# Performance work log

Hardware: AMD Instinct MI355X
Metric: run time of the kernel (lower is better)

The kernel has to match this reference:

```python
import jax, jax.numpy as jnp
import numpy as np

N_NODES = 100000
N_EDGES = 1200000
D_IN = 64
D_OUT = 32
BN_EPS = 1e-5


def setup_inputs() -> dict:
    key = jax.random.key(0)
    ks = jax.random.split(key, 8)
    x = jax.random.normal(ks[0], (N_NODES, D_IN), dtype=jnp.float32)
    edge_index = jax.random.randint(ks[1], (2, N_EDGES), 0, N_NODES, dtype=jnp.int64)
    W1s = jax.random.normal(ks[2], (3, D_IN, D_IN), dtype=jnp.float32) * 0.05
    b1s = jax.random.normal(ks[3], (3, D_IN), dtype=jnp.float32) * 0.05
    W2s = jax.random.normal(ks[4], (3, D_IN, D_IN), dtype=jnp.float32) * 0.05
    b2s = jax.random.normal(ks[5], (3, D_IN), dtype=jnp.float32) * 0.05
    gammas = jnp.ones((3, D_IN), dtype=jnp.float32)
    betas = jnp.zeros((3, D_IN), dtype=jnp.float32)
    epss = jnp.zeros((3,), dtype=jnp.float32)  # GINConv train_eps init value 0
    lin_w = jax.random.normal(ks[6], (D_IN, D_OUT), dtype=jnp.float32) * 0.05
    lin_b = jnp.zeros((D_OUT,), dtype=jnp.float32)
    return {"x": x, "edge_index": edge_index, "W1s": W1s, "b1s": b1s,
            "W2s": W2s, "b2s": b2s, "gammas": gammas, "betas": betas,
            "epss": epss, "lin_w": lin_w, "lin_b": lin_b}


def reference(x, edge_index, W1s, b1s, W2s, b2s, gammas, betas, epss, lin_w, lin_b):
    # PyG GINConv (source_to_target): out_i = nn((1+eps)*x_i + sum_{j->i} x_j)
    src = edge_index[0]
    dst = edge_index[1]
    n = x.shape[0]
    h = x
    for i in range(3):
        agg = jax.ops.segment_sum(h[src], dst, num_segments=n)  # [N, d]
        z = (1.0 + epss[i]) * h + agg
        z = jax.nn.relu(z @ W1s[i] + b1s[i])
        z = jax.nn.relu(z @ W2s[i] + b2s[i])
        # BatchNorm1d, training mode (batch statistics, biased variance)
        mu = jnp.mean(z, axis=0)
        var = jnp.var(z, axis=0)
        z = gammas[i] * (z - mu) * jax.lax.rsqrt(var + BN_EPS) + betas[i]
        h = jax.nn.relu(z)  # F.relu after each conv
    return h @ lin_w + lin_b  # [N, D_OUT]
```

## Files before the change

### kernel.cpp

```cpp
#include <hip/hip_runtime.h>
#include <hip/hip_fp16.h>
#include <hip/hip_cooperative_groups.h>

#define NBMAX 256
#define BCAP  8192
#define CHB   3584

typedef _Float16 half8 __attribute__((ext_vector_type(8)));
typedef float f32x4 __attribute__((ext_vector_type(4)));

__device__ __forceinline__ unsigned short f2h(float f) {
    __half h = __float2half_rn(f);
    return *(unsigned short*)&h;
}

__device__ __forceinline__ int scan256(int v, int* wsum, int* woff) {
    int t = threadIdx.x, lane = t & 63, wv = t >> 6;
    int x = v;
    #pragma unroll
    for (int d = 1; d < 64; d <<= 1) {
        int y = __shfl_up(x, d, 64);
        if (lane >= d) x += y;
    }
    if (lane == 63) wsum[wv] = x;
    __syncthreads();
    if (t == 0) {
        int a = 0;
        #pragma unroll
        for (int i = 0; i < 4; ++i) { woff[i] = a; a += wsum[i]; }
    }
    __syncthreads();
    return x - v + woff[wv];
}

__global__ __launch_bounds__(256) void gin_prep(const float* __restrict__ x,
                                                unsigned short* __restrict__ o, int n16,
                                                const void* __restrict__ edge,
                                                int* __restrict__ gcount,
                                                uint2* __restrict__ ebuf,
                                                int E, int nb, int nbin) {
    if ((int)blockIdx.x >= nbin) {
        int i = (blockIdx.x - nbin) * 256 + threadIdx.x;
        if (i >= n16) return;
        float4 v = ((const float4*)x)[i];
        ushort4 u;
        u.x = f2h(v.x); u.y = f2h(v.y); u.z = f2h(v.z); u.w = f2h(v.w);
        ((ushort4*)o)[i] = u;
        return;
    }
    __shared__ int cnt[NBMAX];
    __shared__ int dlt[NBMAX];
    __shared__ int cur[NBMAX];
    __shared__ int wsum[4], woff[4];
    __shared__ int s_is64;
    __shared__ uint2 buf[CHB];
    int t = threadIdx.x;
    int beg = blockIdx.x * CHB;
    int m = E - beg; if (m > CHB) m = CHB;
    if (t < nb) cnt[t] = 0;
    if (t == 0) s_is64 = 1;
    __syncthreads();
    {
        int m2 = (E < 64) ? E : 64;
        if (t < m2 && ((const int*)edge)[2 * t + 1] != 0) s_is64 = 0;
    }
    __syncthreads();
    int is64 = s_is64;
    for (int j = t; j < m; j += 256) {
        int e = beg + j;
        int d = is64 ? (int)((const long long*)edge)[E + e] : ((const int*)edge)[E + e];
        atomicAdd(&cnt[d >> 9], 1);
    }
    __syncthreads();
    int v = (t < nb) ? cnt[t] : 0;
    int excl = scan256(v, wsum, woff);
    if (t < nb) {
        int gb = v ? atomicAdd(&gcount[t], v) : 0;
        dlt[t] = t * BCAP + gb - excl;
        cur[t] = excl;
    }
    __syncthreads();
    for (int j = t; j < m; j += 256) {
        int e = beg + j;
        int s, d;
        if (is64) {
            s = (int)((const long long*)edge)[e];
            d = (int)((const long long*)edge)[E + e];
        } else {
            s = ((const int*)edge)[e];
            d = ((const int*)edge)[E + e];
        }
        int p = atomicAdd(&cur[d >> 9], 1);
        buf[p] = make_uint2((unsigned)s, (unsigned)d);
    }
    __syncthreads();
    for (int j = t; j < m; j += 256) {
        uint2 ed = buf[j];
        ebuf[j + dlt[(int)(ed.y >> 9)]] = ed;
    }
}

__global__ __launch_bounds__(256) void gin_build(const uint2* __restrict__ ebuf,
                                                 const int* __restrict__ gcount,
                                                 int* __restrict__ rowbeg,
                                                 int* __restrict__ rowend,
                                                 int* __restrict__ col, int n) {
    __shared__ int cnt[512];
    __shared__ int off[512];
    __shared__ int wsum[4], woff[4];
    int b = blockIdx.x, t = threadIdx.x;
    int beg = b * BCAP;
    int end = beg + gcount[b];
    cnt[t] = 0; cnt[t + 256] = 0;
    __syncthreads();
    for (int j = beg + t; j < end; j += 256)
        atomicAdd(&cnt[(int)(ebuf[j].y & 511)], 1);
    __syncthreads();
    int v0 = cnt[2 * t], v1 = cnt[2 * t + 1];
    int ep = scan256(v0 + v1, wsum, woff);
    off[2 * t] = ep;
    off[2 * t + 1] = ep + v0;
    __syncthreads();
    int node0 = b * 512 + 2 * t;
    if (node0 < n) {
        rowbeg[node0] = beg + off[2 * t];
        rowend[node0] = beg + off[2 * t] + v0;
    }
    if (node0 + 1 < n) {
        rowbeg[node0 + 1] = beg + off[2 * t + 1];
        rowend[node0 + 1] = beg + off[2 * t + 1] + v1;
    }
    __syncthreads();
    for (int j = beg + t; j < end; j += 256) {
        uint2 ed = ebuf[j];
        int p = atomicAdd(&off[(int)(ed.y & 511)], 1);
        col[beg + p] = (int)ed.x;
    }
}

template <bool APPLY>
__device__ __forceinline__ void accum8(float* acc, uint4 u,
                                       const float* sc, const float* sh) {
    float v[8];
    float2 f;
    f = __half22float2(*(const __half2*)&u.x); v[0] = f.x; v[1] = f.y;
    f = __half22float2(*(const __half2*)&u.y); v[2] = f.x; v[3] = f.y;
    f = __half22float2(*(const __half2*)&u.z); v[4] = f.x; v[5] = f.y;
    f = __half22float2(*(const __half2*)&u.w); v[6] = f.x; v[7] = f.y;
    #pragma unroll
    for (int j = 0; j < 8; ++j)
        acc[j] += APPLY ? fmaxf(fmaf(v[j], sc[j], sh[j]), 0.f) : v[j];
}

template <bool APPLY>
__device__ __forceinline__ void gather_node(const unsigned short* __restrict__ zb,
                                            int r0, int r1, int ci0,
                                            const int* __restrict__ col,
                                            float e1,
                                            const float* sc, const float* sh,
                                            _Float16* __restrict__ trow,
                                            int wid, int qn, int l16) {
    int r = l16 >> 3, c = l16 & 7;
    uint4 su = make_uint4(0, 0, 0, 0);
    if (r == 0) su = *(const uint4*)(zb + (size_t)wid * 64 + 8 * c);

    float acc[8] = {0.f, 0.f, 0.f, 0.f, 0.f, 0.f, 0.f, 0.f};
    int ci = ci0;
    for (int b2 = r0; b2 < r1; b2 += 16) {
        if (b2 > r0) {
            int ce = b2 + l16;
            ci = col[ce < r1 ? ce : r1 - 1];
        }
        uint4 u[8];
        bool p[8];
        #pragma unroll
        for (int s = 0; s < 8; ++s) {
            int j = 2 * s + r;
            p[s] = (b2 + j) < r1;
            int idx = __shfl(ci, 16 * qn + j);
            if (p[s]) u[s] = *(const uint4*)(zb + (size_t)idx * 64 + 8 * c);
        }
        #pragma unroll
        for (int s = 0; s < 8; ++s)
            if (p[s]) accum8<APPLY>(acc, u[s], sc, sh);
    }
    #pragma unroll
    for (int j = 0; j < 8; ++j)
        acc[j] += __shfl_xor(acc[j], 8);
    if (r == 0) {
        float s[8];
        float2 f;
        f = __half22float2(*(const __half2*)&su.x); s[0] = f.x; s[1] = f.y;
        f = __half22float2(*(const __half2*)&su.y); s[2] = f.x; s[3] = f.y;
        f = __half22float2(*(const __half2*)&su.z); s[4] = f.x; s[5] = f.y;
        f = __half22float2(*(const __half2*)&su.w); s[6] = f.x; s[7] = f.y;
        #pragma unroll
        for (int j = 0; j < 8; ++j) {
            float v = APPLY ? fmaxf(fmaf(s[j], sc[j], sh[j]), 0.f) : s[j];
            acc[j] = fmaf(e1, v, acc[j]);
        }
        uint4 o;
        o.x = (unsigned)f2h(acc[0]) | ((unsigned)f2h(acc[1]) << 16);
        o.y = (unsigned)f2h(acc[2]) | ((unsigned)f2h(acc[3]) << 16);
        o.z = (unsigned)f2h(acc[4]) | ((unsigned)f2h(acc[5]) << 16);
        o.w = (unsigned)f2h(acc[6]) | ((unsigned)f2h(acc[7]) << 16);
        *(uint4*)(trow + 8 * c) = o;
    }
}

template <bool APPLY, bool FINAL>
__global__ __launch_bounds__(512, 4) void gin_fused(const unsigned short* __restrict__ zb,
                                                    const int* __restrict__ rowbeg,
                                                    const int* __restrict__ rowend,
                                                    const int* __restrict__ col,
                                                    const float* __restrict__ epss,
                                                    const float* __restrict__ gammas,
                                                    const float* __restrict__ betas,
                                                    float fN,
                                                    unsigned short* __restrict__ z16,
                                                    const float* __restrict__ W1g,
                                                    const float* __restrict__ b1g,
                                                    const float* __restrict__ W2g,
                                                    const float* __restrict__ b2g,
                                                    float* __restrict__ stats,
                                                    int layer, int n,
                                                    const float* __restrict__ lw,
                                                    const float* __restrict__ lb,
                                                    float* __restrict__ out) {
    __shared__ _Float16 Wt[2 * 64 * 72];
    __shared__ _Float16 Tz[128 * 72];
    __shared__ float sS[64], sQ[64];
    __shared__ float sBN[128];
    int tid = threadIdx.x;
    int base = blockIdx.x * 128;
    const float* __restrict__ W1 = W1g + layer * 4096;
    const float* __restrict__ W2 = W2g + layer * 4096;

    for (int i = tid; i < 4096; i += 512) {
        int k = i >> 6, nn = i & 63;
        Wt[nn * 72 + k]        = (_Float16)W1[i];
        Wt[4608 + nn * 72 + k] = (_Float16)W2[i];
    }
    if (tid < 64) {
        sS[tid] = 0.f; sQ[tid] = 0.f;
        if (APPLY) {
            float mu  = stats[(layer - 1) * 128 + tid] / fN;
            float var = stats[(layer - 1) * 128 + 64 + tid] / fN - mu * mu;
            float g   = gammas[(layer - 1) * 64 + tid];
            float grs = g * rsqrtf(var + 1e-5f);
            sBN[tid]      = grs;
            sBN[64 + tid] = betas[(layer - 1) * 64 + tid] - grs * mu;
        }
    }
    __syncthreads();

    int lane = tid & 63, wv = tid >> 6;
    int qn = lane >> 4;
    int l16 = lane & 15;
    int c8 = l16 & 7;
    float e1 = 1.f + epss[layer];
    float sc[8] = {1.f, 1.f, 1.f, 1.f, 1.f, 1.f, 1.f, 1.f};
    float sh[8] = {0.f, 0.f, 0.f, 0.f, 0.f, 0.f, 0.f, 0.f};
    if (APPLY) {
        *(float4*)&sc[0] = *(const float4*)&sBN[8 * c8];
        *(float4*)&sc[4] = *(const float4*)&sBN[8 * c8 + 4];
        *(float4*)&sh[0] = *(const float4*)&sBN[64 + 8 * c8];
        *(float4*)&sh[4] = *(const float4*)&sBN[64 + 8 * c8 + 4];
    }

    int wvq = wv * 4 + qn;
    int cr0, cr1, pr0, pr1;
    {
        int w0 = base + wvq;
        cr0 = 0; cr1 = 0;
        if (w0 < n) { cr0 = rowbeg[w0]; cr1 = rowend[w0]; }
        int w1 = w0 + 32;
        pr0 = 0; pr1 = 0;
        if (w1 < n) { pr0 = rowbeg[w1]; pr1 = rowend[w1]; }
    }
    int cci = 0;
    if (cr1 > cr0) { int ce = cr0 + l16; cci = col[ce < cr1 ? ce : cr1 - 1]; }
    #pragma unroll 1
    for (int p = 0; p < 4; ++p) {
        int nci = 0;
        if (pr1 > pr0) { int ce = pr0 + l16; nci = col[ce < pr1 ? ce : pr1 - 1]; }
        int fr0 = 0, fr1 = 0;
        {
            int w2 = base + (p + 2) * 32 + wvq;
            if (p < 2 && w2 < n) { fr0 = rowbeg[w2]; fr1 = rowend[w2]; }
        }
        int widl = p * 32 + wvq;
        int wid = base + widl;
        if (wid < n) {
            gather_node<APPLY>(zb, cr0, cr1, cci, col, e1, sc, sh,
                               Tz + widl * 72, wid, qn, l16);
        } else if (l16 < 8) {
            *(uint4*)(Tz + widl * 72 + 8 * c8) = make_uint4(0u, 0u, 0u, 0u);
        }
        cr0 = pr0; cr1 = pr1; cci = nci;
        pr0 = fr0; pr1 = fr1;
    }
    __syncthreads();

    int g = qn, q = l16;
    int n0 = 16 * wv + q;

    half8 tb0 = *(const half8*)&Tz[n0 * 72 + 8 * g];
    half8 tb1 = *(const half8*)&Tz[n0 * 72 + 32 + 8 * g];

    f32x4 acc[4];
    #pragma unroll
    for (int ft = 0; ft < 4; ++ft)
        acc[ft] = (f32x4){0.f, 0.f, 0.f, 0.f};

    #pragma unroll
    for (int ft = 0; ft < 4; ++ft) {
        half8 a0 = *(const half8*)&Wt[(16 * ft + q) * 72 + 8 * g];
        half8 a1 = *(const half8*)&Wt[(16 * ft + q) * 72 + 32 + 8 * g];
        acc[ft] = __builtin_amdgcn_mfma_f32_16x16x32_f16(a0, tb0, acc[ft], 0, 0, 0);
        acc[ft] = __builtin_amdgcn_mfma_f32_16x16x32_f16(a1, tb1, acc[ft], 0, 0, 0);
    }

    #pragma unroll
    for (int ft = 0; ft < 4; ++ft) {
        float4 b = *(const float4*)(b1g + layer * 64 + 16 * ft + 4 * g);
        float v0 = fmaxf(acc[ft][0] + b.x, 0.f);
        float v1 = fmaxf(acc[ft][1] + b.y, 0.f);
        float v2 = fmaxf(acc[ft][2] + b.z, 0.f);
        float v3 = fmaxf(acc[ft][3] + b.w, 0.f);
        uint2 pk;
        pk.x = (unsigned)f2h(v0) | ((unsigned)f2h(v1) << 16);
        pk.y = (unsigned)f2h(v2) | ((unsigned)f2h(v3) << 16);
        *(uint2*)&Tz[n0 * 72 + 16 * ft + 4 * g] = pk;
    }

    half8 zb0 = *(const half8*)&Tz[n0 * 72 + 8 * g];
    half8 zb1 = *(const half8*)&Tz[n0 * 72 + 32 + 8 * g];
    #pragma unroll
    for (int ft = 0; ft < 4; ++ft)
        acc[ft] = (f32x4){0.f, 0.f, 0.f, 0.f};
    #pragma unroll
    for (int ft = 0; ft < 4; ++ft) {
        half8 a0 = *(const half8*)&Wt[4608 + (16 * ft + q) * 72 + 8 * g];
        half8 a1 = *(const half8*)&Wt[4608 + (16 * ft + q) * 72 + 32 + 8 * g];
        acc[ft] = __builtin_amdgcn_mfma_f32_16x16x32_f16(a0, zb0, acc[ft], 0, 0, 0);
        acc[ft] = __builtin_amdgcn_mfma_f32_16x16x32_f16(a1, zb1, acc[ft], 0, 0, 0);
    }

    int nodeg = base + n0;
    #pragma unroll
    for (int ft = 0; ft < 4; ++ft) {
        float4 b = *(const float4*)(b2g + layer * 64 + 16 * ft + 4 * g);
        float v0 = fmaxf(acc[ft][0] + b.x, 0.f);
        float v1 = fmaxf(acc[ft][1] + b.y, 0.f);
        float v2 = fmaxf(acc[ft][2] + b.z, 0.f);
        float v3 = fmaxf(acc[ft][3] + b.w, 0.f);
        float s[4], sq[4];
        bool ok = nodeg < n;
        s[0] = ok ? v0 : 0.f; sq[0] = ok ? v0 * v0 : 0.f;
        s[1] = ok ? v1 : 0.f; sq[1] = ok ? v1 * v1 : 0.f;
        s[2] = ok ? v2 : 0.f; sq[2] = ok ? v2 * v2 : 0.f;
        s[3] = ok ? v3 : 0.f; sq[3] = ok ? v3 * v3 : 0.f;
        uint2 pk;
        pk.x = (unsigned)f2h(v0) | ((unsigned)f2h(v1) << 16);
        pk.y = (unsigned)f2h(v2) | ((unsigned)f2h(v3) << 16);
        *(uint2*)&Tz[n0 * 72 + 16 * ft + 4 * g] = pk;
        #pragma unroll
        for (int off = 1; off < 16; off <<= 1) {
            #pragma unroll
            for (int r2 = 0; r2 < 4; ++r2) {
                s[r2] += __shfl_xor(s[r2], off);
                sq[r2] += __shfl_xor(sq[r2], off);
            }
        }
        if (q == 0) {
            #pragma unroll
            for (int r2 = 0; r2 < 4; ++r2) {
                atomicAdd(&sS[16 * ft + 4 * g + r2], s[r2]);
                atomicAdd(&sQ[16 * ft + 4 * g + r2], sq[r2]);
            }
        }
    }

    if constexpr (!FINAL) {
        #pragma unroll
        for (int t2 = 0; t2 < 2; ++t2) {
            int u = lane + 64 * t2;
            int rloc = 16 * wv + (u >> 3);
            int node = base + rloc;
            if (node < n) {
                uint4 v = *(const uint4*)&Tz[rloc * 72 + (u & 7) * 8];
                *(uint4*)(z16 + (size_t)node * 64 + (u & 7) * 8) = v;
            }
        }
        __syncthreads();
        if (tid < 64) {
            atomicAdd(&stats[layer * 128 + tid], sS[tid]);
            atomicAdd(&stats[layer * 128 + 64 + tid], sQ[tid]);
        }
    } else {
        __syncthreads();
        if (tid < 64) {
            atomicAdd(&stats[layer * 128 + tid], sS[tid]);
            atomicAdd(&stats[layer * 128 + 64 + tid], sQ[tid]);
        }
        __threadfence();
        cooperative_groups::this_grid().sync();

        float* Wl = (float*)Wt;
        for (int i = tid; i < 2048; i += 512) Wl[i] = lw[i];
        if (tid < 64) {
            float mu  = stats[layer * 128 + tid] / fN;
            float var = stats[layer * 128 + 64 + tid] / fN - mu * mu;
            float g2  = gammas[layer * 64 + tid];
            float grs = g2 * rsqrtf(var + 1e-5f);
            sBN[tid]      = grs;
            sBN[64 + tid] = betas[layer * 64 + tid] - grs * mu;
        }
        __syncthreads();

        int tx = tid & 7, ty = tid >> 3;
        float accL[2][4];
        {
            float4 b = *(const float4*)(lb + 4 * tx);
            #pragma unroll
            for (int r = 0; r < 2; ++r) {
                accL[r][0] = b.x; accL[r][1] = b.y; accL[r][2] = b.z; accL[r][3] = b.w;
            }
        }
        #pragma unroll 4
        for (int k = 0; k < 64; ++k) {
            float4 w2 = *(const float4*)&Wl[k * 32 + 4 * tx];
            float s_ = sBN[k], h_ = sBN[64 + k];
            #pragma unroll
            for (int r = 0; r < 2; ++r) {
                int row = ty + 64 * r;
                float zv = (float)Tz[row * 72 + k];
                float a = fmaxf(fmaf(zv, s_, h_), 0.f);
                accL[r][0] = fmaf(a, w2.x, accL[r][0]);
                accL[r][1] = fmaf(a, w2.y, accL[r][1]);
                accL[r][2] = fmaf(a, w2.z, accL[r][2]);
                accL[r][3] = fmaf(a, w2.w, accL[r][3]);
            }
        }
        #pragma unroll
        for (int r = 0; r < 2; ++r) {
            int row = base + ty + 64 * r;
            if (row < n) {
                float4 v;
                v.x = accL[r][0]; v.y = accL[r][1]; v.z = accL[r][2]; v.w = accL[r][3];
                *(float4*)(out + (size_t)row * 32 + 4 * tx) = v;
            }
        }
    }
}

__global__ __launch_bounds__(256) void gin_lin(const unsigned short* __restrict__ zin,
                                               const float* __restrict__ stats,
                                               const float* __restrict__ gammas,
                                               const float* __restrict__ betas,
                                               float fN,
                                               const float* __restrict__ lw,
                                               const float* __restrict__ lb,
                                               float* __restrict__ out, int n) {
    __shared__ float Z[128 * 68];
    int tid = threadIdx.x;
    int base = blockIdx.x * 128;
    int cq = (tid & 15) * 4;
    float4 sc4, sh4;
    {
        float t0[4], t1[4];
        #pragma unroll
        for (int j = 0; j < 4; ++j) {
            int f = cq + j;
            float mu  = stats[256 + f] / fN;
            float var = stats[256 + 64 + f] / fN - mu * mu;
            float g   = gammas[128 + f];
            float grs = g * rsqrtf(var + 1e-5f);
            t0[j] = grs;
            t1[j] = betas[128 + f] - grs * mu;
        }
        sc4 = make_float4(t0[0], t0[1], t0[2], t0[3]);
        sh4 = make_float4(t1[0], t1[1], t1[2], t1[3]);
    }
    {
        const ushort4* __restrict__ src = (const ushort4*)(zin + (size_t)base * 64);
        #pragma unroll
        for (int it = 0; it < 8; ++it) {
            int idx4 = it * 256 + tid;
            int row = idx4 >> 4, c = (idx4 & 15) * 4;
            float4 v = make_float4(0.f, 0.f, 0.f, 0.f);
            if (base + row < n) {
                ushort4 u = src[idx4];
                float2 f0 = __half22float2(*(const __half2*)&u.x);
                float2 f1 = __half22float2(*(const __half2*)&u.z);
                v = make_float4(f0.x, f0.y, f1.x, f1.y);
            }
            float4 r;
            r.x = fmaxf(fmaf(v.x, sc4.x, sh4.x), 0.f);
            r.y = fmaxf(fmaf(v.y, sc4.y, sh4.y), 0.f);
            r.z = fmaxf(fmaf(v.z, sc4.z, sh4.z), 0.f);
            r.w = fmaxf(fmaf(v.w, sc4.w, sh4.w), 0.f);
            *(float4*)&Z[row * 68 + c] = r;
        }
    }
    __syncthreads();
    int tx = tid & 7, ty = tid >> 3;
    float acc[4][4];
    {
        float4 b = *(const float4*)(lb + 4 * tx);
        #pragma unroll
        for (int r = 0; r < 4; ++r) {
            acc[r][0] = b.x; acc[r][1] = b.y; acc[r][2] = b.z; acc[r][3] = b.w;
        }
    }
    #pragma unroll 4
    for (int k = 0; k < 64; ++k) {
        float4 w = *(const float4*)(lw + k * 32 + 4 * tx);
        #pragma unroll
        for (int r = 0; r < 4; ++r) {
            float a = Z[(ty + 32 * r) * 68 + k];
            acc[r][0] = fmaf(a, w.x, acc[r][0]);
            acc[r][1] = fmaf(a, w.y, acc[r][1]);
            acc[r][2] = fmaf(a, w.z, acc[r][2]);
            acc[r][3] = fmaf(a, w.w, acc[r][3]);
        }
    }
    #pragma unroll
    for (int r = 0; r < 4; ++r) {
        int row = base + ty + 32 * r;
        if (row < n) {
            float4 v;
            v.x = acc[r][0]; v.y = acc[r][1]; v.z = acc[r][2]; v.w = acc[r][3];
            *(float4*)(out + (size_t)row * 32 + 4 * tx) = v;
        }
    }
}

extern "C" void kernel_launch(void* const* d_in, const int* in_sizes, int n_in,
                              void* d_out, int out_size, void* d_ws, size_t ws_size,
                              hipStream_t stream) {
    const float* x      = (const float*)d_in[0];
    const void*  edge   = d_in[1];
    const float* W1s    = (const float*)d_in[2];
    const float* b1s    = (const float*)d_in[3];
    const float* W2s    = (const float*)d_in[4];
    const float* b2s    = (const float*)d_in[5];
    const float* gammas = (const float*)d_in[6];
    const float* betas  = (const float*)d_in[7];
    const float* epss   = (const float*)d_in[8];
    const float* lin_w  = (const float*)d_in[9];
    const float* lin_b  = (const float*)d_in[10];
    float* out = (float*)d_out;

    const int N = in_sizes[0] / 64;
    const int E = in_sizes[1] / 2;
    const int NB = (N + 511) >> 9;
    const float fN = (float)N;

    char* w = (char*)d_ws;
    auto take = [&](size_t bytes) {
        char* p = w;
        w += (bytes + 255) & ~(size_t)255;
        return p;
    };
    unsigned short* x16 = (unsigned short*)take((size_t)N * 64 * 2);
    unsigned short* hA  = (unsigned short*)take((size_t)N * 64 * 2);
    unsigned short* hB  = (unsigned short*)take((size_t)N * 64 * 2);
    uint2* ebuf    = (uint2*)take((size_t)NB * BCAP * 8);
    int*   col     = (int*)take((size_t)NB * BCAP * 4);
    int*   rowbeg  = (int*)take((size_t)N * 4);
    int*   rowend  = (int*)take((size_t)N * 4);
    int*   gcount  = (int*)take((size_t)NBMAX * 4);
    float* stats   = (float*)take(3 * 128 * 4);

    hipMemsetAsync(gcount, 0, 1024 + 1536, stream);

    const int n16 = N * 16;
    const int nbin = (E + CHB - 1) / CHB;
    const int gx = (n16 + 255) / 256;
    gin_prep<<<nbin + gx, 256, 0, stream>>>(x, x16, n16, edge, gcount, ebuf, E, NB, nbin);
    gin_build<<<NB, 256, 0, stream>>>(ebuf, gcount, rowbeg, rowend, col, N);

    const int gMlp = (N + 127) / 128;

    gin_fused<false, false><<<gMlp, 512, 0, stream>>>(x16, rowbeg, rowend, col, epss,
                                                      gammas, betas, fN, hA,
                                                      W1s, b1s, W2s, b2s, stats, 0, N,
                                                      nullptr, nullptr, nullptr);
    gin_fused<true, false><<<gMlp, 512, 0, stream>>>(hA, rowbeg, rowend, col, epss,
                                                     gammas, betas, fN, hB,
                                                     W1s, b1s, W2s, b2s, stats, 1, N,
                                                     nullptr, nullptr, nullptr);

    bool coop = false;
    {
        int dev = 0;
        hipGetDevice(&dev);
        int numCU = 0;
        hipDeviceGetAttribute(&numCU, hipDeviceAttributeMultiprocessorCount, dev);
        int maxB = 0;
        hipOccupancyMaxActiveBlocksPerMultiprocessor(
            &maxB, reinterpret_cast<const void*>(&gin_fused<true, true>), 512, 0);
        if (maxB > 0 && numCU > 0 && (long long)maxB * numCU >= (long long)gMlp)
            coop = true;
    }
    if (coop) {
        const unsigned short* zi = hB;
        unsigned short* zo = hA;
        int Lv = 2, Nv = N;
        float fNv = fN;
        void* args[] = {
            (void*)&zi, (void*)&rowbeg, (void*)&rowend, (void*)&col,
            (void*)&epss, (void*)&gammas, (void*)&betas, (void*)&fNv,
            (void*)&zo, (void*)&W1s, (void*)&b1s, (void*)&W2s, (void*)&b2s,
            (void*)&stats, (void*)&Lv, (void*)&Nv,
            (void*)&lin_w, (void*)&lin_b, (void*)&out
        };
        hipError_t err = hipLaunchCooperativeKernel(
            reinterpret_cast<const void*>(&gin_fused<true, true>),
            dim3(gMlp), dim3(512), args, 0, stream);
        if (err != hipSuccess) coop = false;
    }
    if (!coop) {
        gin_fused<true, false><<<gMlp, 512, 0, stream>>>(hB, rowbeg, rowend, col, epss,
                                                         gammas, betas, fN, hA,
                                                         W1s, b1s, W2s, b2s, stats, 2, N,
                                                         nullptr, nullptr, nullptr);
        gin_lin<<<gMlp, 256, 0, stream>>>(hA, stats, gammas, betas, fN, lin_w, lin_b, out, N);
    }
}
```

Baseline: 301.2 us.

## Fuse all three GIN layers and final linear into one persistent megakernel

Replaces the three per-layer kernel launches plus the cooperative final launch with a single persistent kernel. It loops over the layers and separates them with a custom atomic grid barrier in global memory, in place of cooperative-groups grid sync. The aim is to remove launch gaps and per-layer kernel tails. The barrier relies on every block being co-resident under a plain launch, checked only via an occupancy query, and launch_bounds is raised to 8 blocks per CU, which may constrain registers.

```diff
diff --git a/kernel.cpp b/kernel.cpp
--- a/kernel.cpp
+++ b/kernel.cpp
@@ -1,6 +1,5 @@
 #include <hip/hip_runtime.h>
 #include <hip/hip_fp16.h>
-#include <hip/hip_cooperative_groups.h>
 
 #define NBMAX 256
 #define BCAP  8192
@@ -208,7 +207,172 @@
     }
 }
 
-template <bool APPLY, bool FINAL>
+template <bool APPLY>
+__device__ __forceinline__ void gin_layer(const unsigned short* __restrict__ zb,
+                                          const int* __restrict__ rowbeg,
+                                          const int* __restrict__ rowend,
+                                          const int* __restrict__ col,
+                                          float e1,
+                                          const float* __restrict__ b1,
+                                          const float* __restrict__ b2,
+                                          float* __restrict__ statsL,
+                                          _Float16* __restrict__ Wt,
+                                          _Float16* __restrict__ Tz,
+                                          float* __restrict__ sS,
+                                          float* __restrict__ sQ,
+                                          const float* __restrict__ sBN,
+                                          int base, int n) {
+    int tid = threadIdx.x;
+    int lane = tid & 63, wv = tid >> 6;
+    int qn = lane >> 4;
+    int l16 = lane & 15;
+    int c8 = l16 & 7;
+    float sc[8] = {1.f, 1.f, 1.f, 1.f, 1.f, 1.f, 1.f, 1.f};
+    float sh[8] = {0.f, 0.f, 0.f, 0.f, 0.f, 0.f, 0.f, 0.f};
+    if (APPLY) {
+        *(float4*)&sc[0] = *(const float4*)&sBN[8 * c8];
+        *(float4*)&sc[4] = *(const float4*)&sBN[8 * c8 + 4];
+        *(float4*)&sh[0] = *(const float4*)&sBN[64 + 8 * c8];
+        *(float4*)&sh[4] = *(const float4*)&sBN[64 + 8 * c8 + 4];
+    }
+
+    int wvq = wv * 4 + qn;
+    int cr0, cr1, pr0, pr1;
+    {
+        int w0 = base + wvq;
+        cr0 = 0; cr1 = 0;
+        if (w0 < n) { cr0 = rowbeg[w0]; cr1 = rowend[w0]; }
+        int w1 = w0 + 32;
+        pr0 = 0; pr1 = 0;
+        if (w1 < n) { pr0 = rowbeg[w1]; pr1 = rowend[w1]; }
+    }
+    int cci = 0;
+    if (cr1 > cr0) { int ce = cr0 + l16; cci = col[ce < cr1 ? ce : cr1 - 1]; }
+    #pragma unroll 1
+    for (int p = 0; p < 4; ++p) {
+        int nci = 0;
+        if (pr1 > pr0) { int ce = pr0 + l16; nci = col[ce < pr1 ? ce : pr1 - 1]; }
+        int fr0 = 0, fr1 = 0;
+        {
+            int w2 = base + (p + 2) * 32 + wvq;
+            if (p < 2 && w2 < n) { fr0 = rowbeg[w2]; fr1 = rowend[w2]; }
+        }
+        int widl = p * 32 + wvq;
+        int wid = base + widl;
+        if (wid < n) {
+            gather_node<APPLY>(zb, cr0, cr1, cci, col, e1, sc, sh,
+                               Tz + widl * 72, wid, qn, l16);
+        } else if (l16 < 8) {
+            *(uint4*)(Tz + widl * 72 + 8 * c8) = make_uint4(0u, 0u, 0u, 0u);
+        }
+        cr0 = pr0; cr1 = pr1; cci = nci;
+        pr0 = fr0; pr1 = fr1;
+    }
+    __syncthreads();
+
+    int g = qn, q = l16;
+    int n0 = 16 * wv + q;
+
+    half8 tb0 = *(const half8*)&Tz[n0 * 72 + 8 * g];
+    half8 tb1 = *(const half8*)&Tz[n0 * 72 + 32 + 8 * g];
+
+    f32x4 acc[4];
+    #pragma unroll
+    for (int ft = 0; ft < 4; ++ft)
+        acc[ft] = (f32x4){0.f, 0.f, 0.f, 0.f};
+
+    #pragma unroll
+    for (int ft = 0; ft < 4; ++ft) {
+        half8 a0 = *(const half8*)&Wt[(16 * ft + q) * 72 + 8 * g];
+        half8 a1 = *(const half8*)&Wt[(16 * ft + q) * 72 + 32 + 8 * g];
+        acc[ft] = __builtin_amdgcn_mfma_f32_16x16x32_f16(a0, tb0, acc[ft], 0, 0, 0);
+        acc[ft] = __builtin_amdgcn_mfma_f32_16x16x32_f16(a1, tb1, acc[ft], 0, 0, 0);
+    }
+
+    #pragma unroll
+    for (int ft = 0; ft < 4; ++ft) {
+        float4 b = *(const float4*)(b1 + 16 * ft + 4 * g);
+        float v0 = fmaxf(acc[ft][0] + b.x, 0.f);
+        float v1 = fmaxf(acc[ft][1] + b.y, 0.f);
+        float v2 = fmaxf(acc[ft][2] + b.z, 0.f);
+        float v3 = fmaxf(acc[ft][3] + b.w, 0.f);
+        uint2 pk;
+        pk.x = (unsigned)f2h(v0) | ((unsigned)f2h(v1) << 16);
+        pk.y = (unsigned)f2h(v2) | ((unsigned)f2h(v3) << 16);
+        *(uint2*)&Tz[n0 * 72 + 16 * ft + 4 * g] = pk;
+    }
+
+    half8 zb0 = *(const half8*)&Tz[n0 * 72 + 8 * g];
+    half8 zb1 = *(const half8*)&Tz[n0 * 72 + 32 + 8 * g];
+    #pragma unroll
+    for (int ft = 0; ft < 4; ++ft)
+        acc[ft] = (f32x4){0.f, 0.f, 0.f, 0.f};
+    #pragma unroll
+    for (int ft = 0; ft < 4; ++ft) {
+        half8 a0 = *(const half8*)&Wt[4608 + (16 * ft + q) * 72 + 8 * g];
+        half8 a1 = *(const half8*)&Wt[4608 + (16 * ft + q) * 72 + 32 + 8 * g];
+        acc[ft] = __builtin_amdgcn_mfma_f32_16x16x32_f16(a0, zb0, acc[ft], 0, 0, 0);
+        acc[ft] = __builtin_amdgcn_mfma_f32_16x16x32_f16(a1, zb1, acc[ft], 0, 0, 0);
+    }
+
+    int nodeg = base + n0;
+    #pragma unroll
+    for (int ft = 0; ft < 4; ++ft) {
+        float4 b = *(const float4*)(b2 + 16 * ft + 4 * g);
+        float v0 = fmaxf(acc[ft][0] + b.x, 0.f);
+        float v1 = fmaxf(acc[ft][1] + b.y, 0.f);
+        float v2 = fmaxf(acc[ft][2] + b.z, 0.f);
+        float v3 = fmaxf(acc[ft][3] + b.w, 0.f);
+        float s[4], sq[4];
+        bool ok = nodeg < n;
+        s[0] = ok ? v0 : 0.f; sq[0] = ok ? v0 * v0 : 0.f;
+        s[1] = ok ? v1 : 0.f; sq[1] = ok ? v1 * v1 : 0.f;
+        s[2] = ok ? v2 : 0.f; sq[2] = ok ? v2 * v2 : 0.f;
+        s[3] = ok ? v3 : 0.f; sq[3] = ok ? v3 * v3 : 0.f;
+        uint2 pk;
+        pk.x = (unsigned)f2h(v0) | ((unsigned)f2h(v1) << 16);
+        pk.y = (unsigned)f2h(v2) | ((unsigned)f2h(v3) << 16);
+        *(uint2*)&Tz[n0 * 72 + 16 * ft + 4 * g] = pk;
+        #pragma unroll
+        for (int off = 1; off < 16; off <<= 1) {
+            #pragma unroll
+            for (int r2 = 0; r2 < 4; ++r2) {
+                s[r2] += __shfl_xor(s[r2], off);
+                sq[r2] += __shfl_xor(sq[r2], off);
+            }
+        }
+        if (q == 0) {
+            #pragma unroll
+            for (int r2 = 0; r2 < 4; ++r2) {
+                atomicAdd(&sS[16 * ft + 4 * g + r2], s[r2]);
+                atomicAdd(&sQ[16 * ft + 4 * g + r2], sq[r2]);
+            }
+        }
+    }
+    __syncthreads();
+    if (tid < 64) {
+        atomicAdd(&statsL[tid], sS[tid]);
+        atomicAdd(&statsL[64 + tid], sQ[tid]);
+    }
+}
+
+__device__ __forceinline__ void copyout_z16(const _Float16* __restrict__ Tz,
+                                            unsigned short* __restrict__ z16,
+                                            int base, int n) {
+    int lane = threadIdx.x & 63, wv = threadIdx.x >> 6;
+    #pragma unroll
+    for (int t2 = 0; t2 < 2; ++t2) {
+        int u = lane + 64 * t2;
+        int rloc = 16 * wv + (u >> 3);
+        int node = base + rloc;
+        if (node < n) {
+            uint4 v = *(const uint4*)&Tz[rloc * 72 + (u & 7) * 8];
+            *(uint4*)(z16 + (size_t)node * 64 + (u & 7) * 8) = v;
+        }
+    }
+}
+
+template <bool APPLY>
 __global__ __launch_bounds__(512, 4) void gin_fused(const unsigned short* __restrict__ zb,
                                                     const int* __restrict__ rowbeg,
                                                     const int* __restrict__ rowend,
@@ -223,10 +387,7 @@
                                                     const float* __restrict__ W2g,
                                                     const float* __restrict__ b2g,
                                                     float* __restrict__ stats,
-                                                    int layer, int n,
-                                                    const float* __restrict__ lw,
-                                                    const float* __restrict__ lb,
-                                                    float* __restrict__ out) {
+                                                    int layer, int n) {
     __shared__ _Float16 Wt[2 * 64 * 72];
     __shared__ _Float16 Tz[128 * 72];
     __shared__ float sS[64], sQ[64];
@@ -235,7 +396,6 @@
     int base = blockIdx.x * 128;
     const float* __restrict__ W1 = W1g + layer * 4096;
     const float* __restrict__ W2 = W2g + layer * 4096;
-
     for (int i = tid; i < 4096; i += 512) {
         int k = i >> 6, nn = i & 63;
         Wt[nn * 72 + k]        = (_Float16)W1[i];
@@ -253,204 +413,125 @@
         }
     }
     __syncthreads();
-
-    int lane = tid & 63, wv = tid >> 6;
-    int qn = lane >> 4;
-    int l16 = lane & 15;
-    int c8 = l16 & 7;
-    float e1 = 1.f + epss[layer];
-    float sc[8] = {1.f, 1.f, 1.f, 1.f, 1.f, 1.f, 1.f, 1.f};
-    float sh[8] = {0.f, 0.f, 0.f, 0.f, 0.f, 0.f, 0.f, 0.f};
-    if (APPLY) {
-        *(float4*)&sc[0] = *(const float4*)&sBN[8 * c8];
-        *(float4*)&sc[4] = *(const float4*)&sBN[8 * c8 + 4];
-        *(float4*)&sh[0] = *(const float4*)&sBN[64 + 8 * c8];
-        *(float4*)&sh[4] = *(const float4*)&sBN[64 + 8 * c8 + 4];
-    }
-
-    int wvq = wv * 4 + qn;
-    int cr0, cr1, pr0, pr1;
+    gin_layer<APPLY>(zb, rowbeg, rowend, col, 1.f + epss[layer],
+                     b1g + layer * 64, b2g + layer * 64, stats + layer * 128,
+                     Wt, Tz, sS, sQ, sBN, base, n);
+    copyout_z16(Tz, z16, base, n);
+}
+
+__device__ __forceinline__ void megabar(int* __restrict__ bar, int target) {
+    __syncthreads();
+    if (threadIdx.x == 0) {
+        __threadfence();
+        __hip_atomic_fetch_add(bar, 1, __ATOMIC_RELEASE, __HIP_MEMORY_SCOPE_AGENT);
+        while (__hip_atomic_load(bar, __ATOMIC_ACQUIRE, __HIP_MEMORY_SCOPE_AGENT) < target)
+            __builtin_amdgcn_s_sleep(16);
+    }
+    __syncthreads();
+    __threadfence();
+}
+
+__global__ __launch_bounds__(512, 8) void gin_mega(const unsigned short* __restrict__ x16,
+                                                   unsigned short* __restrict__ hA,
+                                                   unsigned short* __restrict__ hB,
+                                                   const int* __restrict__ rowbeg,
+                                                   const int* __restrict__ rowend,
+                                                   const int* __restrict__ col,
+                                                   const float* __restrict__ epss,
+                                                   const float* __restrict__ gammas,
+                                                   const float* __restrict__ betas,
+                                                   float fN,
+                                                   const float* __restrict__ W1g,
+                                                   const float* __restrict__ b1g,
+                                                   const float* __restrict__ W2g,
+                                                   const float* __restrict__ b2g,
+                                                   float* __restrict__ stats, int n,
+                                                   const float* __restrict__ lw,
+                                                   const float* __restrict__ lb,
+                                                   float* __restrict__ out,
+                                                   int* __restrict__ bar, int nblocks) {
+    __shared__ _Float16 Wt[2 * 64 * 72];
+    __shared__ _Float16 Tz[128 * 72];
+    __shared__ float sS[64], sQ[64];
+    __shared__ float sBN[128];
+    int tid = threadIdx.x;
+    int base = blockIdx.x * 128;
+
+    #pragma unroll 1
+    for (int L = 0; L < 3; ++L) {
+        const unsigned short* zb = (L == 0) ? x16 : ((L == 1) ? hA : hB);
+        const float* W1 = W1g + L * 4096;
+        const float* W2 = W2g + L * 4096;
+        for (int i = tid; i < 4096; i += 512) {
+            int k = i >> 6, nn = i & 63;
+            Wt[nn * 72 + k]        = (_Float16)W1[i];
+            Wt[4608 + nn * 72 + k] = (_Float16)W2[i];
+        }
+        if (tid < 64) {
+            sS[tid] = 0.f; sQ[tid] = 0.f;
+            if (L > 0) {
+                float mu  = stats[(L - 1) * 128 + tid] / fN;
+                float var = stats[(L - 1) * 128 + 64 + tid] / fN - mu * mu;
+                float g   = gammas[(L - 1) * 64 + tid];
+                float grs = g * rsqrtf(var + 1e-5f);
+                sBN[tid]      = grs;
+                sBN[64 + tid] = betas[(L - 1) * 64 + tid] - grs * mu;
+            }
+        }
+        __syncthreads();
+        float e1 = 1.f + epss[L];
+        if (L > 0)
+            gin_layer<true>(zb, rowbeg, rowend, col, e1, b1g + L * 64, b2g + L * 64,
+                            stats + L * 128, Wt, Tz, sS, sQ, sBN, base, n);
+        else
+            gin_layer<false>(zb, rowbeg, rowend, col, e1, b1g, b2g,
+                             stats, Wt, Tz, sS, sQ, sBN, base, n);
+        if (L < 2) copyout_z16(Tz, (L == 0) ? hA : hB, base, n);
+        megabar(bar, nblocks * (L + 1));
+    }
+
+    float* Wl = (float*)Wt;
+    for (int i = tid; i < 2048; i += 512) Wl[i] = lw[i];
+    if (tid < 64) {
+        float mu  = stats[256 + tid] / fN;
+        float var = stats[256 + 64 + tid] / fN - mu * mu;
+        float g2  = gammas[128 + tid];
+        float grs = g2 * rsqrtf(var + 1e-5f);
+        sBN[tid]      = grs;
+        sBN[64 + tid] = betas[128 + tid] - grs * mu;
+    }
+    __syncthreads();
+    int tx = tid & 7, ty = tid >> 3;
+    float accL[2][4];
     {
-        int w0 = base + wvq;
-        cr0 = 0; cr1 = 0;
-        if (w0 < n) { cr0 = rowbeg[w0]; cr1 = rowend[w0]; }
-        int w1 = w0 + 32;
-        pr0 = 0; pr1 = 0;
-        if (w1 < n) { pr0 = rowbeg[w1]; pr1 = rowend[w1]; }
-    }
-    int cci = 0;
-    if (cr1 > cr0) { int ce = cr0 + l16; cci = col[ce < cr1 ? ce : cr1 - 1]; }
-    #pragma unroll 1
-    for (int p = 0; p < 4; ++p) {
-        int nci = 0;
-        if (pr1 > pr0) { int ce = pr0 + l16; nci = col[ce < pr1 ? ce : pr1 - 1]; }
-        int fr0 = 0, fr1 = 0;
-        {
-            int w2 = base + (p + 2) * 32 + wvq;
-            if (p < 2 && w2 < n) { fr0 = rowbeg[w2]; fr1 = rowend[w2]; }
-        }
-        int widl = p * 32 + wvq;
-        int wid = base + widl;
-        if (wid < n) {
-            gather_node<APPLY>(zb, cr0, cr1, cci, col, e1, sc, sh,
-                               Tz + widl * 72, wid, qn, l16);
-        } else if (l16 < 8) {
-            *(uint4*)(Tz + widl * 72 + 8 * c8) = make_uint4(0u, 0u, 0u, 0u);
-        }
-        cr0 = pr0; cr1 = pr1; cci = nci;
-        pr0 = fr0; pr1 = fr1;
-    }
-    __syncthreads();
-
-    int g = qn, q = l16;
-    int n0 = 16 * wv + q;
-
-    half8 tb0 = *(const half8*)&Tz[n0 * 72 + 8 * g];
-    half8 tb1 = *(const half8*)&Tz[n0 * 72 + 32 + 8 * g];
-
-    f32x4 acc[4];
-    #pragma unroll
-    for (int ft = 0; ft < 4; ++ft)
-        acc[ft] = (f32x4){0.f, 0.f, 0.f, 0.f};
-
-    #pragma unroll
-    for (int ft = 0; ft < 4; ++ft) {
-        half8 a0 = *(const half8*)&Wt[(16 * ft + q) * 72 + 8 * g];
-        half8 a1 = *(const half8*)&Wt[(16 * ft + q) * 72 + 32 + 8 * g];
-        acc[ft] = __builtin_amdgcn_mfma_f32_16x16x32_f16(a0, tb0, acc[ft], 0, 0, 0);
-        acc[ft] = __builtin_amdgcn_mfma_f32_16x16x32_f16(a1, tb1, acc[ft], 0, 0, 0);
-    }
-
-    #pragma unroll
-    for (int ft = 0; ft < 4; ++ft) {
-        float4 b = *(const float4*)(b1g + layer * 64 + 16 * ft + 4 * g);
-        float v0 = fmaxf(acc[ft][0] + b.x, 0.f);
-        float v1 = fmaxf(acc[ft][1] + b.y, 0.f);
-        float v2 = fmaxf(acc[ft][2] + b.z, 0.f);
-        float v3 = fmaxf(acc[ft][3] + b.w, 0.f);
-        uint2 pk;
-        pk.x = (unsigned)f2h(v0) | ((unsigned)f2h(v1) << 16);
-        pk.y = (unsigned)f2h(v2) | ((unsigned)f2h(v3) << 16);
-        *(uint2*)&Tz[n0 * 72 + 16 * ft + 4 * g] = pk;
-    }
-
-    half8 zb0 = *(const half8*)&Tz[n0 * 72 + 8 * g];
-    half8 zb1 = *(const half8*)&Tz[n0 * 72 + 32 + 8 * g];
-    #pragma unroll
-    for (int ft = 0; ft < 4; ++ft)
-        acc[ft] = (f32x4){0.f, 0.f, 0.f, 0.f};
-    #pragma unroll
-    for (int ft = 0; ft < 4; ++ft) {
-        half8 a0 = *(const half8*)&Wt[4608 + (16 * ft + q) * 72 + 8 * g];
-        half8 a1 = *(const half8*)&Wt[4608 + (16 * ft + q) * 72 + 32 + 8 * g];
-        acc[ft] = __builtin_amdgcn_mfma_f32_16x16x32_f16(a0, zb0, acc[ft], 0, 0, 0);
-        acc[ft] = __builtin_amdgcn_mfma_f32_16x16x32_f16(a1, zb1, acc[ft], 0, 0, 0);
-    }
-
-    int nodeg = base + n0;
-    #pragma unroll
-    for (int ft = 0; ft < 4; ++ft) {
-        float4 b = *(const float4*)(b2g + layer * 64 + 16 * ft + 4 * g);
-        float v0 = fmaxf(acc[ft][0] + b.x, 0.f);
-        float v1 = fmaxf(acc[ft][1] + b.y, 0.f);
-        float v2 = fmaxf(acc[ft][2] + b.z, 0.f);
-        float v3 = fmaxf(acc[ft][3] + b.w, 0.f);
-        float s[4], sq[4];
-        bool ok = nodeg < n;
-        s[0] = ok ? v0 : 0.f; sq[0] = ok ? v0 * v0 : 0.f;
-        s[1] = ok ? v1 : 0.f; sq[1] = ok ? v1 * v1 : 0.f;
-        s[2] = ok ? v2 : 0.f; sq[2] = ok ? v2 * v2 : 0.f;
-        s[3] = ok ? v3 : 0.f; sq[3] = ok ? v3 * v3 : 0.f;
-        uint2 pk;
-        pk.x = (unsigned)f2h(v0) | ((unsigned)f2h(v1) << 16);
-        pk.y = (unsigned)f2h(v2) | ((unsigned)f2h(v3) << 16);
-        *(uint2*)&Tz[n0 * 72 + 16 * ft + 4 * g] = pk;
-        #pragma unroll
-        for (int off = 1; off < 16; off <<= 1) {
-            #pragma unroll
-            for (int r2 = 0; r2 < 4; ++r2) {
-                s[r2] += __shfl_xor(s[r2], off);
-                sq[r2] += __shfl_xor(sq[r2], off);
-            }
-        }
-        if (q == 0) {
-            #pragma unroll
-            for (int r2 = 0; r2 < 4; ++r2) {
-                atomicAdd(&sS[16 * ft + 4 * g + r2], s[r2]);
-                atomicAdd(&sQ[16 * ft + 4 * g + r2], sq[r2]);
-            }
-        }
-    }
-
-    if constexpr (!FINAL) {
-        #pragma unroll
-        for (int t2 = 0; t2 < 2; ++t2) {
-            int u = lane + 64 * t2;
-            int rloc = 16 * wv + (u >> 3);
-            int node = base + rloc;
-            if (node < n) {
-                uint4 v = *(const uint4*)&Tz[rloc * 72 + (u & 7) * 8];
-                *(uint4*)(z16 + (size_t)node * 64 + (u & 7) * 8) = v;
-            }
-        }
-        __syncthreads();
-        if (tid < 64) {
-            atomicAdd(&stats[layer * 128 + tid], sS[tid]);
-            atomicAdd(&stats[layer * 128 + 64 + tid], sQ[tid]);
-        }
-    } else {
-        __syncthreads();
-        if (tid < 64) {
-            atomicAdd(&stats[layer * 128 + tid], sS[tid]);
-            atomicAdd(&stats[layer * 128 + 64 + tid], sQ[tid]);
-        }
-        __threadfence();
-        cooperative_groups::this_grid().sync();
-
-        float* Wl = (float*)Wt;
-        for (int i = tid; i < 2048; i += 512) Wl[i] = lw[i];
-        if (tid < 64) {
-            float mu  = stats[layer * 128 + tid] / fN;
-            float var = stats[layer * 128 + 64 + tid] / fN - mu * mu;
-            float g2  = gammas[layer * 64 + tid];
-            float grs = g2 * rsqrtf(var + 1e-5f);
-            sBN[tid]      = grs;
-            sBN[64 + tid] = betas[layer * 64 + tid] - grs * mu;
-        }
-        __syncthreads();
-
-        int tx = tid & 7, ty = tid >> 3;
-        float accL[2][4];
-        {
-            float4 b = *(const float4*)(lb + 4 * tx);
-            #pragma unroll
-            for (int r = 0; r < 2; ++r) {
-                accL[r][0] = b.x; accL[r][1] = b.y; accL[r][2] = b.z; accL[r][3] = b.w;
-            }
-        }
-        #pragma unroll 4
-        for (int k = 0; k < 64; ++k) {
-            float4 w2 = *(const float4*)&Wl[k * 32 + 4 * tx];
-            float s_ = sBN[k], h_ = sBN[64 + k];
-            #pragma unroll
-            for (int r = 0; r < 2; ++r) {
-                int row = ty + 64 * r;
-                float zv = (float)Tz[row * 72 + k];
-                float a = fmaxf(fmaf(zv, s_, h_), 0.f);
-                accL[r][0] = fmaf(a, w2.x, accL[r][0]);
-                accL[r][1] = fmaf(a, w2.y, accL[r][1]);
-                accL[r][2] = fmaf(a, w2.z, accL[r][2]);
-                accL[r][3] = fmaf(a, w2.w, accL[r][3]);
-            }
-        }
+        float4 b = *(const float4*)(lb + 4 * tx);
         #pragma unroll
         for (int r = 0; r < 2; ++r) {
-            int row = base + ty + 64 * r;
-            if (row < n) {
-                float4 v;
-                v.x = accL[r][0]; v.y = accL[r][1]; v.z = accL[r][2]; v.w = accL[r][3];
-                *(float4*)(out + (size_t)row * 32 + 4 * tx) = v;
-            }
+            accL[r][0] = b.x; accL[r][1] = b.y; accL[r][2] = b.z; accL[r][3] = b.w;
+        }
+    }
+    #pragma unroll 4
+    for (int k = 0; k < 64; ++k) {
+        float4 w2 = *(const float4*)&Wl[k * 32 + 4 * tx];
+        float s_ = sBN[k], h_ = sBN[64 + k];
+        #pragma unroll
+        for (int r = 0; r < 2; ++r) {
+            int row = ty + 64 * r;
+            float zv = (float)Tz[row * 72 + k];
+            float a = fmaxf(fmaf(zv, s_, h_), 0.f);
+            accL[r][0] = fmaf(a, w2.x, accL[r][0]);
+            accL[r][1] = fmaf(a, w2.y, accL[r][1]);
+            accL[r][2] = fmaf(a, w2.z, accL[r][2]);
+            accL[r][3] = fmaf(a, w2.w, accL[r][3]);
+        }
+    }
+    #pragma unroll
+    for (int r = 0; r < 2; ++r) {
+        int row = base + ty + 64 * r;
+        if (row < n) {
+            float4 v;
+            v.x = accL[r][0]; v.y = accL[r][1]; v.z = accL[r][2]; v.w = accL[r][3];
+            *(float4*)(out + (size_t)row * 32 + 4 * tx) = v;
         }
     }
 }
@@ -573,8 +654,9 @@
     int*   rowend  = (int*)take((size_t)N * 4);
     int*   gcount  = (int*)take((size_t)NBMAX * 4);
     float* stats   = (float*)take(3 * 128 * 4);
-
-    hipMemsetAsync(gcount, 0, 1024 + 1536, stream);
+    int*   bar     = (int*)take(256);
+
+    hipMemsetAsync(gcount, 0, 1024 + 1536 + 256, stream);
 
     const int n16 = N * 16;
     const int nbin = (E + CHB - 1) / CHB;
@@ -584,49 +666,31 @@
 
     const int gMlp = (N + 127) / 128;
 
-    gin_fused<false, false><<<gMlp, 512, 0, stream>>>(x16, rowbeg, rowend, col, epss,
-                                                      gammas, betas, fN, hA,
-                                                      W1s, b1s, W2s, b2s, stats, 0, N,
-                                                      nullptr, nullptr, nullptr);
-    gin_fused<true, false><<<gMlp, 512, 0, stream>>>(hA, rowbeg, rowend, col, epss,
-                                                     gammas, betas, fN, hB,
-                                                     W1s, b1s, W2s, b2s, stats, 1, N,
-                                                     nullptr, nullptr, nullptr);
-
-    bool coop = false;
+    bool mega = false;
     {
         int dev = 0;
         hipGetDevice(&dev);
         int numCU = 0;
         hipDeviceGetAttribute(&numCU, hipDeviceAttributeMultiprocessorCount, dev);
         int maxB = 0;
-        hipOccupancyMaxActiveBlocksPerMultiprocessor(
-            &maxB, reinterpret_cast<const void*>(&gin_fused<true, true>), 512, 0);
+        hipOccupancyMaxActiveBlocksPerMultiprocessor(&maxB, gin_mega, 512, 0);
         if (maxB > 0 && numCU > 0 && (long long)maxB * numCU >= (long long)gMlp)
-            coop = true;
-    }
-    if (coop) {
-        const unsigned short* zi = hB;
-        unsigned short* zo = hA;
-        int Lv = 2, Nv = N;
-        float fNv = fN;
-        void* args[] = {
-            (void*)&zi, (void*)&rowbeg, (void*)&rowend, (void*)&col,
-            (void*)&epss, (void*)&gammas, (void*)&betas, (void*)&fNv,
-            (void*)&zo, (void*)&W1s, (void*)&b1s, (void*)&W2s, (void*)&b2s,
-            (void*)&stats, (void*)&Lv, (void*)&Nv,
-            (void*)&lin_w, (void*)&lin_b, (void*)&out
-        };
-        hipError_t err = hipLaunchCooperativeKernel(
-            reinterpret_cast<const void*>(&gin_fused<true, true>),
-            dim3(gMlp), dim3(512), args, 0, stream);
-        if (err != hipSuccess) coop = false;
-    }
-    if (!coop) {
-        gin_fused<true, false><<<gMlp, 512, 0, stream>>>(hB, rowbeg, rowend, col, epss,
-                                                         gammas, betas, fN, hA,
-                                                         W1s, b1s, W2s, b2s, stats, 2, N,
-                                                         nullptr, nullptr, nullptr);
+            mega = true;
+    }
+    if (mega) {
+        gin_mega<<<gMlp, 512, 0, stream>>>(x16, hA, hB, rowbeg, rowend, col, epss,
+                                           gammas, betas, fN, W1s, b1s, W2s, b2s,
+                                           stats, N, lin_w, lin_b, out, bar, gMlp);
+    } else {
+        gin_fused<false><<<gMlp, 512, 0, stream>>>(x16, rowbeg, rowend, col, epss,
+                                                   gammas, betas, fN, hA,
+                                                   W1s, b1s, W2s, b2s, stats, 0, N);
+        gin_fused<true><<<gMlp, 512, 0, stream>>>(hA, rowbeg, rowend, col, epss,
+                                                  gammas, betas, fN, hB,
+                                                  W1s, b1s, W2s, b2s, stats, 1, N);
+        gin_fused<true><<<gMlp, 512, 0, stream>>>(hB, rowbeg, rowend, col, epss,
+                                                  gammas, betas, fN, hA,
+                                                  W1s, b1s, W2s, b2s, stats, 2, N);
         gin_lin<<<gMlp, 256, 0, stream>>>(hA, stats, gammas, betas, fN, lin_w, lin_b, out, N);
     }
 }
```

Result: no change. 304.0 us (+0.9%).
